# Kernel optimization log

Hardware: AMD Instinct MI355X
Metric: run time of the kernel (lower is better)

## Reference

```python
import jax, jax.numpy as jnp
import numpy as np

B, N, DIM = 8, 8192, 512
H, DH = 8, 64
INNER = H * DH
EPS = 1e-5


def setup_inputs() -> dict:
    key = jax.random.key(0)
    ks = jax.random.split(key, 5)
    x = jax.random.normal(ks[0], (B, N, DIM), dtype=jnp.float32)
    w_qkv = jax.random.normal(ks[1], (DIM, 3 * INNER), dtype=jnp.float32) * (DIM ** -0.5)
    ln_w = jnp.ones((INNER,), dtype=jnp.float32)
    ln_b = jnp.zeros((INNER,), dtype=jnp.float32)
    w_out = jax.random.normal(ks[2], (INNER, DIM), dtype=jnp.float32) * (INNER ** -0.5)
    b_out = jnp.zeros((DIM,), dtype=jnp.float32)
    return {"x": x, "w_qkv": w_qkv, "ln_w": ln_w, "ln_b": ln_b,
            "w_out": w_out, "b_out": b_out}


def _layernorm(x, w, b):
    mu = jnp.mean(x, axis=-1, keepdims=True)
    var = jnp.mean(jnp.square(x - mu), axis=-1, keepdims=True)
    return (x - mu) * jax.lax.rsqrt(var + EPS) * w + b


def reference(x, w_qkv, ln_w, ln_b, w_out, b_out):
    b, n, _ = x.shape
    qkv = x @ w_qkv  # [b, n, 3*inner]
    q, k, v = jnp.split(qkv, 3, axis=-1)
    # b n (h d) -> b h n d
    def heads(t):
        return t.reshape(b, n, H, DH).transpose(0, 2, 1, 3)
    q, k, v = heads(q), heads(k), heads(v)
    q = jax.nn.relu(q)
    k = jax.nn.relu(k)
    kv = jnp.einsum('bhnm,bhnd->bhmd', k, v)   # [b, h, d, d]
    out = jnp.einsum('bhnm,bhmd->bhnd', q, kv)  # [b, h, n, d]
    out = out.transpose(0, 2, 1, 3).reshape(b, n, INNER)
    out = _layernorm(out, ln_w, ln_b)
    return out @ w_out + b_out
```

## Files before the change

kernel.cpp:

```cpp
#include <hip/hip_runtime.h>
#include <stdint.h>

#define B_ 8
#define N_ 8192
#define DIM_ 512
#define H_ 8
#define DH_ 64
#define ROWS (B_*N_)
#define TRIPLE (3*DIM_)
#define EPS_ 1e-5f

typedef __attribute__((ext_vector_type(8))) short short8;
typedef __attribute__((ext_vector_type(4))) float f32x4;
typedef __attribute__((ext_vector_type(4))) float fl4;
typedef __attribute__((ext_vector_type(4))) unsigned short us4;
typedef __attribute__((ext_vector_type(8))) unsigned short us8;

#define AS1 __attribute__((address_space(1)))
#define AS3 __attribute__((address_space(3)))

__device__ __forceinline__ void gld16(const void* g, void* l) {
    __builtin_amdgcn_global_load_lds((const AS1 void*)(uintptr_t)g,
                                     (AS3 void*)(unsigned)(uintptr_t)l, 16, 0, 0);
}

__device__ inline unsigned short f2bf(float f) {
    union { float f; unsigned int u; } x; x.f = f;
    unsigned int r = x.u + 0x7fffu + ((x.u >> 16) & 1u);
    return (unsigned short)(r >> 16);
}
__device__ inline float bf2f(unsigned short b) {
    union { unsigned int u; float f; } x; x.u = ((unsigned int)b) << 16;
    return x.f;
}

__device__ __forceinline__ int eoff(int row, int col) {
    return row * 64 + (col ^ ((((unsigned)row >> 2) & 3) << 4));
}

__global__ __launch_bounds__(256) void k_cvt(const float* __restrict__ x,
                                             unsigned short* __restrict__ xb) {
    size_t i = ((size_t)blockIdx.x * 256 + threadIdx.x) * 8;
    fl4 a = *(const fl4*)(x + i);
    fl4 b = *(const fl4*)(x + i + 4);
    us8 r;
    r[0] = f2bf(a[0]); r[1] = f2bf(a[1]); r[2] = f2bf(a[2]); r[3] = f2bf(a[3]);
    r[4] = f2bf(b[0]); r[5] = f2bf(b[1]); r[6] = f2bf(b[2]); r[7] = f2bf(b[3]);
    *(us8*)(xb + i) = r;
}

__global__ void k_prep(const float* __restrict__ w_qkv, const float* __restrict__ w_out,
                       unsigned short* __restrict__ wqkvT, unsigned short* __restrict__ woutT) {
    int idx = blockIdx.x * 256 + threadIdx.x;
    if (idx < TRIPLE * DIM_) {
        int n = idx / DIM_, k = idx - n * DIM_;
        wqkvT[idx] = f2bf(w_qkv[(size_t)k * TRIPLE + n]);
    }
    if (idx < DIM_ * DIM_) {
        int n = idx / DIM_, k = idx - n * DIM_;
        woutT[idx] = f2bf(w_out[(size_t)k * DIM_ + n]);
    }
}

__global__ __launch_bounds__(512, 2) void k_qkv8(const unsigned short* __restrict__ xb,
        const unsigned short* __restrict__ wT,
        unsigned short* __restrict__ qkv)
{
    __shared__ __align__(1024) unsigned short Ab[2][16384];
    __shared__ __align__(1024) unsigned short Bb[2][16384];

    const int tid  = threadIdx.x;
    const int lane = tid & 63;
    const int wid  = tid >> 6;
    const int wr   = wid >> 2;
    const int wc   = wid & 3;
    const int lr   = lane & 15;

    int id  = blockIdx.x;
    int nid = (id & 7) * 192 + (id >> 3);
    int n0  = (nid % 6) * 256;
    int m0  = (nid / 6) * 256;

    const unsigned short* pA[4];
    const unsigned short* pB[4];
    unsigned ldst[4];
#pragma unroll
    for (int j = 0; j < 4; ++j) {
        int s    = tid + j * 512;
        int row  = ((s >> 7) << 4) + ((s >> 2) & 15);
        int colb = ((s & 3) << 4) ^ (((s >> 5) & 1) << 5);
        int col  = ((s >> 6) & 1) * 32 + (colb >> 1);
        pA[j] = xb + (size_t)(m0 + row) * 512 + col;
        pB[j] = wT + (size_t)(n0 + row) * 512 + col;
        ldst[j] = (unsigned)((j * 512 + wid * 64) * 8);
    }
    const int lo = lr * 32 + ((((lane >> 4) << 4) ^ ((lr >> 3) << 5)) >> 1);

    auto STAGE = [&](int t, int c) {
#pragma unroll
        for (int j = 0; j < 4; ++j) {
            gld16(pA[j] + t * 64, (void*)&Ab[c][ldst[j]]);
            gld16(pB[j] + t * 64, (void*)&Bb[c][ldst[j]]);
        }
    };

    f32x4 acc[8][4] = {};
    short8 af[4][2], bf0[2][2], bf1[2][2];

    STAGE(0, 0);
    asm volatile("s_waitcnt vmcnt(0)" ::: "memory");
    __builtin_amdgcn_s_barrier();

    for (int t = 0; t < 8; ++t) {
        const int cur = t & 1;
        const unsigned short* Ac = Ab[cur];
        const unsigned short* Bc = Bb[cur];

        if (t < 7) STAGE(t + 1, cur ^ 1);
#pragma unroll
        for (int m = 0; m < 4; ++m)
#pragma unroll
            for (int ks = 0; ks < 2; ++ks)
                af[m][ks] = *(const short8*)&Ac[(wr * 16 + m * 2 + ks) * 512 + lo];
#pragma unroll
        for (int n = 0; n < 2; ++n)
#pragma unroll
            for (int ks = 0; ks < 2; ++ks)
                bf0[n][ks] = *(const short8*)&Bc[((wc * 4 + n) * 2 + ks) * 512 + lo];
        __builtin_amdgcn_s_barrier();
        __builtin_amdgcn_s_setprio(1);
#pragma unroll
        for (int m = 0; m < 4; ++m)
#pragma unroll
            for (int n = 0; n < 2; ++n)
#pragma unroll
                for (int ks = 0; ks < 2; ++ks)
                    acc[m][n] = __builtin_amdgcn_mfma_f32_16x16x32_bf16(af[m][ks], bf0[n][ks], acc[m][n], 0, 0, 0);
        __builtin_amdgcn_s_setprio(0);
        __builtin_amdgcn_s_barrier();

#pragma unroll
        for (int n = 0; n < 2; ++n)
#pragma unroll
            for (int ks = 0; ks < 2; ++ks)
                bf1[n][ks] = *(const short8*)&Bc[((wc * 4 + 2 + n) * 2 + ks) * 512 + lo];
        __builtin_amdgcn_s_barrier();
        __builtin_amdgcn_s_setprio(1);
#pragma unroll
        for (int m = 0; m < 4; ++m)
#pragma unroll
            for (int n = 0; n < 2; ++n)
#pragma unroll
                for (int ks = 0; ks < 2; ++ks)
                    acc[m][2 + n] = __builtin_amdgcn_mfma_f32_16x16x32_bf16(af[m][ks], bf1[n][ks], acc[m][2 + n], 0, 0, 0);
        __builtin_amdgcn_s_setprio(0);
        __builtin_amdgcn_s_barrier();

#pragma unroll
        for (int m = 0; m < 4; ++m)
#pragma unroll
            for (int ks = 0; ks < 2; ++ks)
                af[m][ks] = *(const short8*)&Ac[(wr * 16 + (4 + m) * 2 + ks) * 512 + lo];
        __builtin_amdgcn_s_barrier();
        __builtin_amdgcn_s_setprio(1);
#pragma unroll
        for (int m = 0; m < 4; ++m)
#pragma unroll
            for (int n = 0; n < 2; ++n)
#pragma unroll
                for (int ks = 0; ks < 2; ++ks)
                    acc[4 + m][2 + n] = __builtin_amdgcn_mfma_f32_16x16x32_bf16(af[m][ks], bf1[n][ks], acc[4 + m][2 + n], 0, 0, 0);
        __builtin_amdgcn_s_setprio(0);
        __builtin_amdgcn_s_barrier();

#pragma unroll
        for (int n = 0; n < 2; ++n)
#pragma unroll
            for (int ks = 0; ks < 2; ++ks)
                bf0[n][ks] = *(const short8*)&Bc[((wc * 4 + n) * 2 + ks) * 512 + lo];
        __builtin_amdgcn_s_barrier();
        __builtin_amdgcn_s_setprio(1);
#pragma unroll
        for (int m = 0; m < 4; ++m)
#pragma unroll
            for (int n = 0; n < 2; ++n)
#pragma unroll
                for (int ks = 0; ks < 2; ++ks)
                    acc[4 + m][n] = __builtin_amdgcn_mfma_f32_16x16x32_bf16(af[m][ks], bf0[n][ks], acc[4 + m][n], 0, 0, 0);
        __builtin_amdgcn_s_setprio(0);
        if (t < 7) asm volatile("s_waitcnt vmcnt(0)" ::: "memory");
        __builtin_amdgcn_s_barrier();
    }

    unsigned short* S = (wid < 4) ? (&Ab[0][0] + wid * 8192)
                                  : (&Bb[0][0] + (wid - 4) * 8192);
    const bool relu_tile = (n0 < 1024);
#pragma unroll
    for (int m = 0; m < 8; ++m) {
        int rbase = m * 16 + ((lane >> 4) << 2);
#pragma unroll
        for (int n = 0; n < 4; ++n) {
            int col = n * 16 + lr;
#pragma unroll
            for (int r = 0; r < 4; ++r) {
                float v = acc[m][n][r];
                if (relu_tile && v < 0.0f) v = 0.0f;
                S[eoff(rbase + r, col)] = f2bf(v);
            }
        }
    }
    __syncthreads();
    {
        int rsub = lane >> 3, sub = lane & 7;
        size_t grow = (size_t)(m0 + wr * 128);
        int gcol = n0 + wc * 64 + sub * 8;
#pragma unroll
        for (int rd = 0; rd < 16; ++rd) {
            int row = rd * 8 + rsub;
            short8 vv = *(const short8*)&S[eoff(row, sub * 8)];
            *(short8*)(qkv + (grow + row) * TRIPLE + gcol) = vv;
        }
    }
}

__global__ __launch_bounds__(256) void k_qkv_f(const float* __restrict__ x,
        const unsigned short* __restrict__ wT,
        unsigned short* __restrict__ qkv)
{
    __shared__ unsigned short As[128][40];
    __shared__ unsigned short Bs[128][40];
    int t = threadIdx.x;
    int lane = t & 63, wave = t >> 6;
    int m0 = blockIdx.y * 128;
    int n0 = blockIdx.x * 128;
    int wm = (wave & 1) * 64, wn = (wave >> 1) * 64;
    int lr = lane & 15, kg = (lane >> 4) * 8;

    f32x4 acc[4][4] = {};
    for (int k0 = 0; k0 < DIM_; k0 += 32) {
#pragma unroll
        for (int i = 0; i < 4; ++i) {
            int c = t + 256 * i;
            int r = c >> 3, c4 = (c & 7) * 4;
            fl4 v = *(const fl4*)(x + (size_t)(m0 + r) * DIM_ + k0 + c4);
            unsigned short* dst = &As[r][c4];
            dst[0] = f2bf(v[0]); dst[1] = f2bf(v[1]); dst[2] = f2bf(v[2]); dst[3] = f2bf(v[3]);
        }
#pragma unroll
        for (int i = 0; i < 2; ++i) {
            int c = t + 256 * i;
            int r = c >> 2, c8 = (c & 3) * 8;
            *(int4*)&Bs[r][c8] = *(const int4*)(wT + (size_t)(n0 + r) * DIM_ + k0 + c8);
        }
        __syncthreads();
        short8 af[4], bfr[4];
#pragma unroll
        for (int i = 0; i < 4; ++i) af[i]  = *(short8*)&As[wm + i*16 + lr][kg];
#pragma unroll
        for (int j = 0; j < 4; ++j) bfr[j] = *(short8*)&Bs[wn + j*16 + lr][kg];
#pragma unroll
        for (int i = 0; i < 4; ++i)
#pragma unroll
            for (int j = 0; j < 4; ++j)
                acc[i][j] = __builtin_amdgcn_mfma_f32_16x16x32_bf16(af[i], bfr[j], acc[i][j], 0, 0, 0);
        __syncthreads();
    }
#pragma unroll
    for (int i = 0; i < 4; ++i) {
        int row = m0 + wm + i*16 + (lane >> 4) * 4;
#pragma unroll
        for (int j = 0; j < 4; ++j) {
            int col = n0 + wn + j*16 + (lane & 15);
            bool rl = (col < 1024);
#pragma unroll
            for (int r = 0; r < 4; ++r) {
                float v = acc[i][j][r];
                if (rl && v < 0.0f) v = 0.0f;
                qkv[(size_t)(row + r) * TRIPLE + col] = f2bf(v);
            }
        }
    }
}

__global__ __launch_bounds__(256) void k_kv(const unsigned short* __restrict__ qkv,
                                            float* __restrict__ kv)
{
    __shared__ unsigned short KT[64][136];
    __shared__ unsigned short VT[64][136];
    __shared__ float red[64 * 64];
    int t = threadIdx.x, lane = t & 63, wave = t >> 6;
    int bh = blockIdx.x;
    int b = bh >> 3, h = bh & 7;
    int chunk = blockIdx.y;
    size_t rowbase = (size_t)b * N_ + (size_t)chunk * 1024;
    int kcol = DIM_ + h * 64;
    int vcol = 2 * DIM_ + h * 64;
    int lr = lane & 15;

    f32x4 acc[4][4] = {};
    for (int tile = 0; tile < 8; ++tile) {
        size_t r0 = rowbase + tile * 128;
#pragma unroll
        for (int i = 0; i < 8; ++i) {
            int c = t + 256 * i;
            int r = c >> 4, f4 = (c & 15) * 4;
            us4 kq = *(const us4*)(qkv + (r0 + r) * TRIPLE + kcol + f4);
            us4 vq = *(const us4*)(qkv + (r0 + r) * TRIPLE + vcol + f4);
#pragma unroll
            for (int j = 0; j < 4; ++j) { KT[f4 + j][r] = kq[j]; VT[f4 + j][r] = vq[j]; }
        }
        __syncthreads();
        int kg = wave * 32 + (lane >> 4) * 8;
        short8 af[4], bfr[4];
#pragma unroll
        for (int i = 0; i < 4; ++i) af[i]  = *(short8*)&KT[i*16 + lr][kg];
#pragma unroll
        for (int j = 0; j < 4; ++j) bfr[j] = *(short8*)&VT[j*16 + lr][kg];
#pragma unroll
        for (int i = 0; i < 4; ++i)
#pragma unroll
            for (int j = 0; j < 4; ++j)
                acc[i][j] = __builtin_amdgcn_mfma_f32_16x16x32_bf16(af[i], bfr[j], acc[i][j], 0, 0, 0);
        __syncthreads();
    }
    for (int w = 0; w < 4; ++w) {
        if (wave == w) {
#pragma unroll
            for (int i = 0; i < 4; ++i)
#pragma unroll
                for (int j = 0; j < 4; ++j)
#pragma unroll
                    for (int r = 0; r < 4; ++r) {
                        int m = i*16 + (lane >> 4) * 4 + r;
                        int d = j*16 + (lane & 15);
                        if (w == 0) red[m * 64 + d] = acc[i][j][r];
                        else        red[m * 64 + d] += acc[i][j][r];
                    }
        }
        __syncthreads();
    }
    float* kvout = kv + (size_t)bh * 4096;
#pragma unroll
    for (int i = 0; i < 16; ++i) {
        int idx = t + 256 * i;
        atomicAdd(&kvout[idx], red[idx]);
    }
}

__global__ __launch_bounds__(256) void k_attn(unsigned short* __restrict__ qkv,
                                              const float* __restrict__ kv,
                                              float* __restrict__ rowstats)
{
    __shared__ unsigned short Qh[128][72];
    __shared__ unsigned short kvT[64][72];
    __shared__ __align__(64) unsigned short Sout[128 * 64];
    int t = threadIdx.x, lane = t & 63, wave = t >> 6;
    size_t r0 = (size_t)blockIdx.x * 128;
    int b = (int)(r0 / N_);
    int lr = lane & 15;

    float s8[8] = {}, ss8[8] = {};

    for (int h = 0; h < H_; ++h) {
#pragma unroll
        for (int i = 0; i < 8; ++i) {
            int c = t + 256 * i;
            int r = c >> 4, f4 = (c & 15) * 4;
            *(us4*)&Qh[r][f4] = *(const us4*)(qkv + (r0 + r) * TRIPLE + h * 64 + f4);
        }
        const float* kvh = kv + (size_t)(b * 8 + h) * 4096;
#pragma unroll
        for (int i = 0; i < 16; ++i) {
            int idx = t + 256 * i;
            int m = idx >> 6, d = idx & 63;
            kvT[d][m] = f2bf(kvh[idx]);
        }
        __syncthreads();
        f32x4 acc[2][4] = {};
#pragma unroll
        for (int ks = 0; ks < 2; ++ks) {
            int kg = ks * 32 + (lane >> 4) * 8;
            short8 af[2], bfr[4];
#pragma unroll
            for (int i = 0; i < 2; ++i) af[i]  = *(short8*)&Qh[wave*32 + i*16 + lr][kg];
#pragma unroll
            for (int j = 0; j < 4; ++j) bfr[j] = *(short8*)&kvT[j*16 + lr][kg];
#pragma unroll
            for (int i = 0; i < 2; ++i)
#pragma unroll
                for (int j = 0; j < 4; ++j)
                    acc[i][j] = __builtin_amdgcn_mfma_f32_16x16x32_bf16(af[i], bfr[j], acc[i][j], 0, 0, 0);
        }
#pragma unroll
        for (int i = 0; i < 2; ++i)
#pragma unroll
            for (int j = 0; j < 4; ++j) {
                int rbase = wave*32 + i*16 + (lane >> 4) * 4;
                int col = j*16 + lr;
#pragma unroll
                for (int r = 0; r < 4; ++r) {
                    float v = acc[i][j][r];
                    s8[i*4+r]  += v;
                    ss8[i*4+r] += v * v;
                    Sout[eoff(rbase + r, col)] = f2bf(v);
                }
            }
        __syncthreads();
        {
            int sub = t & 7, rsub = t >> 3;
#pragma unroll
            for (int rd = 0; rd < 4; ++rd) {
                int row = rd * 32 + rsub;
                short8 vv = *(const short8*)&Sout[eoff(row, sub * 8)];
                *(short8*)(qkv + (r0 + row) * TRIPLE + h * 64 + sub * 8) = vv;
            }
        }
        __syncthreads();
    }

#pragma unroll
    for (int q = 0; q < 8; ++q) {
        float s = s8[q], ss = ss8[q];
        s += __shfl_xor(s, 1);  ss += __shfl_xor(ss, 1);
        s += __shfl_xor(s, 2);  ss += __shfl_xor(ss, 2);
        s += __shfl_xor(s, 4);  ss += __shfl_xor(ss, 4);
        s += __shfl_xor(s, 8);  ss += __shfl_xor(ss, 8);
        s8[q] = s; ss8[q] = ss;
    }
    if (lr == 0) {
#pragma unroll
        for (int q = 0; q < 8; ++q) {
            int row = wave*32 + (q >> 2)*16 + (lane >> 4)*4 + (q & 3);
            float m = s8[q] * (1.0f / 512.0f);
            float rs = rsqrtf(ss8[q] * (1.0f / 512.0f) - m * m + EPS_);
            rowstats[2 * (r0 + row)]     = m;
            rowstats[2 * (r0 + row) + 1] = rs;
        }
    }
}

__global__ __launch_bounds__(256) void k_out(const unsigned short* __restrict__ qkv,
        const unsigned short* __restrict__ woutT,
        const float* __restrict__ rowstats,
        const float* __restrict__ lnw, const float* __restrict__ lnb,
        const float* __restrict__ bout, float* __restrict__ out)
{
    __shared__ unsigned short As[128][40];
    __shared__ unsigned short Bs[128][40];
    __shared__ float mu[128], rs[128], lw[512], lb[512];
    int t = threadIdx.x, lane = t & 63, wave = t >> 6;
    int m0 = blockIdx.y * 128, n0 = blockIdx.x * 128;
    int wm = (wave & 1) * 64, wn = (wave >> 1) * 64;
    int lr = lane & 15, kg = (lane >> 4) * 8;

    for (int i = t; i < 512; i += 256) { lw[i] = lnw[i]; lb[i] = lnb[i]; }
    if (t < 128) {
        mu[t] = rowstats[2 * (m0 + t)];
        rs[t] = rowstats[2 * (m0 + t) + 1];
    }
    __syncthreads();

    f32x4 acc[4][4] = {};
    for (int k0 = 0; k0 < 512; k0 += 32) {
#pragma unroll
        for (int i = 0; i < 4; ++i) {
            int c = t + 256 * i;
            int r = c >> 3, c4 = (c & 7) * 4;
            us4 v = *(const us4*)(qkv + (size_t)(m0 + r) * TRIPLE + k0 + c4);
            float mm = mu[r], rr = rs[r];
            unsigned short* dst = &As[r][c4];
#pragma unroll
            for (int j = 0; j < 4; ++j) {
                float f = (bf2f(v[j]) - mm) * rr * lw[k0 + c4 + j] + lb[k0 + c4 + j];
                dst[j] = f2bf(f);
            }
        }
#pragma unroll
        for (int i = 0; i < 2; ++i) {
            int c = t + 256 * i;
            int r = c >> 2, c8 = (c & 3) * 8;
            *(int4*)&Bs[r][c8] = *(const int4*)(woutT + (size_t)(n0 + r) * DIM_ + k0 + c8);
        }
        __syncthreads();
        short8 af[4], bfr[4];
#pragma unroll
        for (int i = 0; i < 4; ++i) af[i]  = *(short8*)&As[wm + i*16 + lr][kg];
#pragma unroll
        for (int j = 0; j < 4; ++j) bfr[j] = *(short8*)&Bs[wn + j*16 + lr][kg];
#pragma unroll
        for (int i = 0; i < 4; ++i)
#pragma unroll
            for (int j = 0; j < 4; ++j)
                acc[i][j] = __builtin_amdgcn_mfma_f32_16x16x32_bf16(af[i], bfr[j], acc[i][j], 0, 0, 0);
        __syncthreads();
    }
#pragma unroll
    for (int i = 0; i < 4; ++i) {
        int row = m0 + wm + i*16 + (lane >> 4) * 4;
#pragma unroll
        for (int j = 0; j < 4; ++j) {
            int col = n0 + wn + j*16 + (lane & 15);
            float bo = bout[col];
#pragma unroll
            for (int r = 0; r < 4; ++r)
                out[(size_t)(row + r) * DIM_ + col] = acc[i][j][r] + bo;
        }
    }
}

extern "C" void kernel_launch(void* const* d_in, const int* in_sizes, int n_in,
                              void* d_out, int out_size, void* d_ws, size_t ws_size,
                              hipStream_t stream) {
    (void)in_sizes; (void)n_in; (void)out_size;
    const float* x     = (const float*)d_in[0];
    const float* w_qkv = (const float*)d_in[1];
    const float* ln_w  = (const float*)d_in[2];
    const float* ln_b  = (const float*)d_in[3];
    const float* w_out = (const float*)d_in[4];
    const float* b_out = (const float*)d_in[5];
    float* out = (float*)d_out;

    char* ws = (char*)d_ws;
    const size_t QKV_BYTES = (size_t)ROWS * TRIPLE * sizeof(unsigned short);
    const size_t KV_BYTES  = (size_t)64 * 64 * 64 * sizeof(float);
    const size_t WQT_BYTES = (size_t)TRIPLE * DIM_ * sizeof(unsigned short);
    const size_t WOT_BYTES = (size_t)DIM_ * DIM_ * sizeof(unsigned short);
    const size_t RS_BYTES  = (size_t)ROWS * 2 * sizeof(float);
    const size_t XB_BYTES  = (size_t)ROWS * DIM_ * sizeof(unsigned short);
    unsigned short* qkv   = (unsigned short*)ws;
    float*          kvbuf = (float*)(ws + QKV_BYTES);
    unsigned short* wqkvT = (unsigned short*)(ws + QKV_BYTES + KV_BYTES);
    unsigned short* woutT = (unsigned short*)(ws + QKV_BYTES + KV_BYTES + WQT_BYTES);
    float*          rstat = (float*)(ws + QKV_BYTES + KV_BYTES + WQT_BYTES + WOT_BYTES);
    unsigned short* xb    = (unsigned short*)(ws + QKV_BYTES + KV_BYTES + WQT_BYTES + WOT_BYTES + RS_BYTES);
    const size_t NEED = QKV_BYTES + KV_BYTES + WQT_BYTES + WOT_BYTES + RS_BYTES + XB_BYTES;

    hipMemsetAsync(kvbuf, 0, KV_BYTES, stream);
    k_prep<<<3072, 256, 0, stream>>>(w_qkv, w_out, wqkvT, woutT);
    if (ws_size >= NEED) {
        k_cvt<<<16384, 256, 0, stream>>>(x, xb);
        k_qkv8<<<dim3(1536), 512, 0, stream>>>(xb, wqkvT, qkv);
    } else {
        k_qkv_f<<<dim3(12, 512), 256, 0, stream>>>(x, wqkvT, qkv);
    }
    k_kv<<<dim3(64, 8), 256, 0, stream>>>(qkv, kvbuf);
    k_attn<<<512, 256, 0, stream>>>(qkv, kvbuf, rstat);
    k_out<<<dim3(4, 512), 256, 0, stream>>>(qkv, woutT, rstat, ln_w, ln_b, b_out, out);
}
```

Measured before the change: 572.7 us.

## Deepen QKV GEMM pipeline to four K=32 stages and tile weight transpose

The QKV GEMM main loop moves from a double-buffered K=64 schedule, with several barriers per iteration, to a 4-slot ring of K=32 stages. Loads run three stages ahead and the loop uses partial vmcnt waits with a single barrier per step, so global loads overlap more with MFMA work and fewer synchronisations are needed. Separately, the weight prep kernel now transposes through a padded 32x33 LDS tile, giving coalesced reads and writes instead of strided scalar reads. Risks include the correctness of the vmcnt counts and the ring-slot reuse, and the smaller per-stage K may give less compute to hide each barrier.

After: 552.5 us. -3.5%, faster.

```diff
diff --git a/kernel.cpp b/kernel.cpp
--- a/kernel.cpp
+++ b/kernel.cpp
@@ -49,25 +49,39 @@
     *(us8*)(xb + i) = r;
 }
 
-__global__ void k_prep(const float* __restrict__ w_qkv, const float* __restrict__ w_out,
-                       unsigned short* __restrict__ wqkvT, unsigned short* __restrict__ woutT) {
-    int idx = blockIdx.x * 256 + threadIdx.x;
-    if (idx < TRIPLE * DIM_) {
-        int n = idx / DIM_, k = idx - n * DIM_;
-        wqkvT[idx] = f2bf(w_qkv[(size_t)k * TRIPLE + n]);
-    }
-    if (idx < DIM_ * DIM_) {
-        int n = idx / DIM_, k = idx - n * DIM_;
-        woutT[idx] = f2bf(w_out[(size_t)k * DIM_ + n]);
-    }
+__global__ __launch_bounds__(256) void k_prep(const float* __restrict__ wq,
+        const float* __restrict__ wo,
+        unsigned short* __restrict__ wqT, unsigned short* __restrict__ woT) {
+    __shared__ float T[32][33];
+    int bid = blockIdx.x;
+    const float* src; unsigned short* dst; int srcCols, dstCols, k0, n0;
+    if (bid < 768) {
+        int tn = bid % 48, tk = bid / 48;
+        src = wq; dst = wqT; srcCols = 1536; dstCols = 512;
+        k0 = tk * 32; n0 = tn * 32;
+    } else {
+        int b = bid - 768;
+        int tn = b % 16, tk = b / 16;
+        src = wo; dst = woT; srcCols = 512; dstCols = 512;
+        k0 = tk * 32; n0 = tn * 32;
+    }
+    int t = threadIdx.x, r = t >> 3, c4 = (t & 7) * 4;
+    fl4 v = *(const fl4*)(src + (size_t)(k0 + r) * srcCols + n0 + c4);
+    T[c4 + 0][r] = v[0]; T[c4 + 1][r] = v[1];
+    T[c4 + 2][r] = v[2]; T[c4 + 3][r] = v[3];
+    __syncthreads();
+    us4 o;
+    o[0] = f2bf(T[r][c4 + 0]); o[1] = f2bf(T[r][c4 + 1]);
+    o[2] = f2bf(T[r][c4 + 2]); o[3] = f2bf(T[r][c4 + 3]);
+    *(us4*)(dst + (size_t)(n0 + r) * dstCols + k0 + c4) = o;
 }
 
 __global__ __launch_bounds__(512, 2) void k_qkv8(const unsigned short* __restrict__ xb,
         const unsigned short* __restrict__ wT,
         unsigned short* __restrict__ qkv)
 {
-    __shared__ __align__(1024) unsigned short Ab[2][16384];
-    __shared__ __align__(1024) unsigned short Bb[2][16384];
+    __shared__ __align__(1024) unsigned short Ab[4][8192];
+    __shared__ __align__(1024) unsigned short Bb[4][8192];
 
     const int tid  = threadIdx.x;
     const int lane = tid & 63;
@@ -81,116 +95,67 @@
     int n0  = (nid % 6) * 256;
     int m0  = (nid / 6) * 256;
 
-    const unsigned short* pA[4];
-    const unsigned short* pB[4];
-    unsigned ldst[4];
-#pragma unroll
-    for (int j = 0; j < 4; ++j) {
+    const unsigned short* pA[2];
+    const unsigned short* pB[2];
+    unsigned ldst[2];
+#pragma unroll
+    for (int j = 0; j < 2; ++j) {
         int s    = tid + j * 512;
-        int row  = ((s >> 7) << 4) + ((s >> 2) & 15);
+        int row  = ((s >> 6) << 4) + ((s >> 2) & 15);
         int colb = ((s & 3) << 4) ^ (((s >> 5) & 1) << 5);
-        int col  = ((s >> 6) & 1) * 32 + (colb >> 1);
+        int col  = colb >> 1;
         pA[j] = xb + (size_t)(m0 + row) * 512 + col;
         pB[j] = wT + (size_t)(n0 + row) * 512 + col;
         ldst[j] = (unsigned)((j * 512 + wid * 64) * 8);
     }
-    const int lo = lr * 32 + ((((lane >> 4) << 4) ^ ((lr >> 3) << 5)) >> 1);
-
-    auto STAGE = [&](int t, int c) {
-#pragma unroll
-        for (int j = 0; j < 4; ++j) {
-            gld16(pA[j] + t * 64, (void*)&Ab[c][ldst[j]]);
-            gld16(pB[j] + t * 64, (void*)&Bb[c][ldst[j]]);
+    const int kg = (lane >> 4) * 8;
+    const int lo = lr * 32 + (kg ^ ((lr >> 3) << 4));
+
+    auto STAGE = [&](int t, int slot) {
+#pragma unroll
+        for (int j = 0; j < 2; ++j) {
+            gld16(pA[j] + t * 32, (void*)&Ab[slot][ldst[j]]);
+            gld16(pB[j] + t * 32, (void*)&Bb[slot][ldst[j]]);
         }
     };
 
     f32x4 acc[8][4] = {};
-    short8 af[4][2], bf0[2][2], bf1[2][2];
+    short8 af[8], bfr[4];
 
     STAGE(0, 0);
-    asm volatile("s_waitcnt vmcnt(0)" ::: "memory");
-    __builtin_amdgcn_s_barrier();
-
-    for (int t = 0; t < 8; ++t) {
-        const int cur = t & 1;
-        const unsigned short* Ac = Ab[cur];
-        const unsigned short* Bc = Bb[cur];
-
-        if (t < 7) STAGE(t + 1, cur ^ 1);
-#pragma unroll
-        for (int m = 0; m < 4; ++m)
-#pragma unroll
-            for (int ks = 0; ks < 2; ++ks)
-                af[m][ks] = *(const short8*)&Ac[(wr * 16 + m * 2 + ks) * 512 + lo];
-#pragma unroll
-        for (int n = 0; n < 2; ++n)
-#pragma unroll
-            for (int ks = 0; ks < 2; ++ks)
-                bf0[n][ks] = *(const short8*)&Bc[((wc * 4 + n) * 2 + ks) * 512 + lo];
+    STAGE(1, 1);
+    STAGE(2, 2);
+
+#define WAITV(n) asm volatile("s_waitcnt vmcnt(" #n ")" ::: "memory")
+#pragma unroll
+    for (int t = 0; t < 16; ++t) {
+        if (t <= 13)      WAITV(8);
+        else if (t == 14) WAITV(4);
+        else              WAITV(0);
         __builtin_amdgcn_s_barrier();
+        __builtin_amdgcn_sched_barrier(0);
+
+        if (t + 3 < 16) STAGE(t + 3, (t + 3) & 3);
+        const unsigned short* Ac = Ab[t & 3];
+        const unsigned short* Bc = Bb[t & 3];
+#pragma unroll
+        for (int m = 0; m < 8; ++m)
+            af[m] = *(const short8*)&Ac[(wr * 8 + m) * 512 + lo];
+#pragma unroll
+        for (int n = 0; n < 4; ++n)
+            bfr[n] = *(const short8*)&Bc[(wc * 4 + n) * 512 + lo];
+
         __builtin_amdgcn_s_setprio(1);
 #pragma unroll
-        for (int m = 0; m < 4; ++m)
-#pragma unroll
-            for (int n = 0; n < 2; ++n)
-#pragma unroll
-                for (int ks = 0; ks < 2; ++ks)
-                    acc[m][n] = __builtin_amdgcn_mfma_f32_16x16x32_bf16(af[m][ks], bf0[n][ks], acc[m][n], 0, 0, 0);
+        for (int m = 0; m < 8; ++m)
+#pragma unroll
+            for (int n = 0; n < 4; ++n)
+                acc[m][n] = __builtin_amdgcn_mfma_f32_16x16x32_bf16(af[m], bfr[n], acc[m][n], 0, 0, 0);
         __builtin_amdgcn_s_setprio(0);
-        __builtin_amdgcn_s_barrier();
-
-#pragma unroll
-        for (int n = 0; n < 2; ++n)
-#pragma unroll
-            for (int ks = 0; ks < 2; ++ks)
-                bf1[n][ks] = *(const short8*)&Bc[((wc * 4 + 2 + n) * 2 + ks) * 512 + lo];
-        __builtin_amdgcn_s_barrier();
-        __builtin_amdgcn_s_setprio(1);
-#pragma unroll
-        for (int m = 0; m < 4; ++m)
-#pragma unroll
-            for (int n = 0; n < 2; ++n)
-#pragma unroll
-                for (int ks = 0; ks < 2; ++ks)
-                    acc[m][2 + n] = __builtin_amdgcn_mfma_f32_16x16x32_bf16(af[m][ks], bf1[n][ks], acc[m][2 + n], 0, 0, 0);
-        __builtin_amdgcn_s_setprio(0);
-        __builtin_amdgcn_s_barrier();
-
-#pragma unroll
-        for (int m = 0; m < 4; ++m)
-#pragma unroll
-            for (int ks = 0; ks < 2; ++ks)
-                af[m][ks] = *(const short8*)&Ac[(wr * 16 + (4 + m) * 2 + ks) * 512 + lo];
-        __builtin_amdgcn_s_barrier();
-        __builtin_amdgcn_s_setprio(1);
-#pragma unroll
-        for (int m = 0; m < 4; ++m)
-#pragma unroll
-            for (int n = 0; n < 2; ++n)
-#pragma unroll
-                for (int ks = 0; ks < 2; ++ks)
-                    acc[4 + m][2 + n] = __builtin_amdgcn_mfma_f32_16x16x32_bf16(af[m][ks], bf1[n][ks], acc[4 + m][2 + n], 0, 0, 0);
-        __builtin_amdgcn_s_setprio(0);
-        __builtin_amdgcn_s_barrier();
-
-#pragma unroll
-        for (int n = 0; n < 2; ++n)
-#pragma unroll
-            for (int ks = 0; ks < 2; ++ks)
-                bf0[n][ks] = *(const short8*)&Bc[((wc * 4 + n) * 2 + ks) * 512 + lo];
-        __builtin_amdgcn_s_barrier();
-        __builtin_amdgcn_s_setprio(1);
-#pragma unroll
-        for (int m = 0; m < 4; ++m)
-#pragma unroll
-            for (int n = 0; n < 2; ++n)
-#pragma unroll
-                for (int ks = 0; ks < 2; ++ks)
-                    acc[4 + m][n] = __builtin_amdgcn_mfma_f32_16x16x32_bf16(af[m][ks], bf0[n][ks], acc[4 + m][n], 0, 0, 0);
-        __builtin_amdgcn_s_setprio(0);
-        if (t < 7) asm volatile("s_waitcnt vmcnt(0)" ::: "memory");
-        __builtin_amdgcn_s_barrier();
-    }
+    }
+#undef WAITV
+
+    __syncthreads();
 
     unsigned short* S = (wid < 4) ? (&Ab[0][0] + wid * 8192)
                                   : (&Bb[0][0] + (wid - 4) * 8192);
@@ -536,7 +501,7 @@
     const size_t NEED = QKV_BYTES + KV_BYTES + WQT_BYTES + WOT_BYTES + RS_BYTES + XB_BYTES;
 
     hipMemsetAsync(kvbuf, 0, KV_BYTES, stream);
-    k_prep<<<3072, 256, 0, stream>>>(w_qkv, w_out, wqkvT, woutT);
+    k_prep<<<1024, 256, 0, stream>>>(w_qkv, w_out, wqkvT, woutT);
     if (ws_size >= NEED) {
         k_cvt<<<16384, 256, 0, stream>>>(x, xb);
         k_qkv8<<<dim3(1536), 512, 0, stream>>>(xb, wqkvT, qkv);
```
